# Kernel optimization log

Measured on AMD Instinct MI355X. Metric: run time of the kernel, lower is better.

The kernel has to match this reference:

```python
import jax, jax.numpy as jnp
from jax import lax
import numpy as np

D = 128          # condition_dim
NUM_STEPS = 1000
FFN = 2048       # torch TransformerEncoderLayer default dim_feedforward


def _conv(x, w, b):
    # 3x3 conv, stride 1, padding 1 (SAME), NCHW / OIHW layout as in torch
    y = lax.conv_general_dilated(x, w, (1, 1), 'SAME',
                                 dimension_numbers=('NCHW', 'OIHW', 'NCHW'))
    return y + b[None, :, None, None]


def _ln(x, g, b):
    m = jnp.mean(x, -1, keepdims=True)
    v = jnp.mean((x - m) ** 2, -1, keepdims=True)
    return (x - m) / jnp.sqrt(v + 1e-5) * g + b


def setup_inputs() -> dict:
    key = jax.random.key(0)
    ks = iter(jax.random.split(key, 40))
    B, C, H, W = 64, 3, 128, 128
    flat = C * H * W
    def rn(shape, scale=0.02):
        return jax.random.normal(next(ks), shape, jnp.float32) * scale
    return dict(
        cond_img=jax.random.normal(next(ks), (B, C, H, W), jnp.float32),
        tgt_img=jax.random.normal(next(ks), (B, C, H, W), jnp.float32),
        noise=jax.random.normal(next(ks), (B, C, H, W), jnp.float32),
        t=jax.random.randint(next(ks), (B,), 0, NUM_STEPS),
        # condition encoder params
        enc_lin_w=rn((D, flat)), enc_lin_b=jnp.zeros((D,), jnp.float32),
        in_w=rn((2, 3 * D, D)), in_b=jnp.zeros((2, 3 * D), jnp.float32),
        out_w=rn((2, D, D)), out_b=jnp.zeros((2, D), jnp.float32),
        ff1_w=rn((2, FFN, D)), ff1_b=jnp.zeros((2, FFN), jnp.float32),
        ff2_w=rn((2, D, FFN)), ff2_b=jnp.zeros((2, D), jnp.float32),
        ln1_g=jnp.ones((2, D), jnp.float32), ln1_b=jnp.zeros((2, D), jnp.float32),
        ln2_g=jnp.ones((2, D), jnp.float32), ln2_b=jnp.zeros((2, D), jnp.float32),
        # SimpleUNet params
        d1_w=rn((32, C, 3, 3)), d1_b=jnp.zeros((32,), jnp.float32),
        d2_w=rn((64, 32, 3, 3)), d2_b=jnp.zeros((64,), jnp.float32),
        mid_w=rn((64, D)), mid_b=jnp.zeros((64,), jnp.float32),
        u1_w=rn((32, 64, 3, 3)), u1_b=jnp.zeros((32,), jnp.float32),
        u2_w=rn((C, 32, 3, 3)), u2_b=jnp.zeros((C,), jnp.float32),
    )


def _forward(cond_img, tgt_img, noise, t,
             enc_lin_w, enc_lin_b, in_w, in_b, out_w, out_b,
             ff1_w, ff1_b, ff2_w, ff2_b, ln1_g, ln1_b, ln2_g, ln2_b,
             d1_w, d1_b, d2_w, d2_b, mid_w, mid_b, u1_w, u1_b, u2_w, u2_b):
    B = cond_img.shape[0]
    # ---- TransformerConditionEncoder (seq_len == 1, eval mode) ----
    x = cond_img.reshape(B, -1) @ enc_lin_w.T + enc_lin_b  # [B, D]
    for i in range(2):
        # self-attention over a length-1 sequence: softmax over one key == 1,
        # so attn(x) == out_proj(v_proj(x)) exactly.
        v = x @ in_w[i][2 * D:3 * D].T + in_b[i][2 * D:3 * D]
        a = v @ out_w[i].T + out_b[i]
        x = _ln(x + a, ln1_g[i], ln1_b[i])
        f = jnp.maximum(x @ ff1_w[i].T + ff1_b[i], 0.0) @ ff2_w[i].T + ff2_b[i]
        x = _ln(x + f, ln2_g[i], ln2_b[i])
    c = x  # [B, D]
    # ---- LinearScheduler.q_sample ----
    betas = jnp.linspace(1e-4, 0.02, NUM_STEPS)
    alpha_bars = jnp.cumprod(1.0 - betas)
    ab = alpha_bars[t][:, None, None, None]
    z_t = jnp.sqrt(ab) * tgt_img + jnp.sqrt(1.0 - ab) * noise
    # ---- SimpleUNet ----
    h = jax.nn.relu(_conv(z_t, d1_w, d1_b))
    h = jax.nn.relu(_conv(h, d2_w, d2_b))
    h = h + (c @ mid_w.T + mid_b)[:, :, None, None]
    h = jax.nn.relu(_conv(h, u1_w, u1_b))
    eps_pred = _conv(h, u2_w, u2_b)
    # ---- MSE loss ----
    return jnp.mean((eps_pred - noise) ** 2)


def reference(cond_img, tgt_img, noise, t,
              enc_lin_w, enc_lin_b, in_w, in_b, out_w, out_b,
              ff1_w, ff1_b, ff2_w, ff2_b, ln1_g, ln1_b, ln2_g, ln2_b,
              d1_w, d1_b, d2_w, d2_b, mid_w, mid_b, u1_w, u1_b, u2_w, u2_b):
    return _forward(cond_img, tgt_img, noise, t,
                    enc_lin_w, enc_lin_b, in_w, in_b, out_w, out_b,
                    ff1_w, ff1_b, ff2_w, ff2_b, ln1_g, ln1_b, ln2_g, ln2_b,
                    d1_w, d1_b, d2_w, d2_b, mid_w, mid_b, u1_w, u1_b, u2_w, u2_b)
```

## Files before the change

kernel.cpp:

```cpp
#include <hip/hip_runtime.h>
#include <math.h>

#define ENC_K 49152
#define KSEG 64
#define KLEN (ENC_K / KSEG)

typedef __attribute__((ext_vector_type(8))) short bf16x8;
typedef __attribute__((ext_vector_type(4))) float f32x4;

__device__ inline unsigned short f2bf(float f) {
    unsigned int u = __builtin_bit_cast(unsigned int, f);
    unsigned int r = u + 0x7fffu + ((u >> 16) & 1u);
    return (unsigned short)(r >> 16);
}
__device__ inline float bf2f(unsigned short h) {
    return __builtin_bit_cast(float, ((unsigned int)h) << 16);
}
__device__ inline float dot4(const float4 a, const float4 b) {
    return a.x * b.x + a.y * b.y + a.z * b.z + a.w * b.w;
}

__global__ void k_alpha(const int* __restrict__ t, float* __restrict__ sab, float* __restrict__ snab) {
    int b = threadIdx.x;
    if (b < 64) {
        int tb = t[b];
        const float step = (0.02f - 1e-4f) / 999.0f;
        float ab = 1.0f;
        for (int i = 0; i <= tb; ++i) {
            float beta = 1e-4f + step * (float)i;
            ab *= (1.0f - beta);
        }
        sab[b] = sqrtf(ab);
        snab[b] = sqrtf(1.0f - ab);
    }
}

__global__ void k_prep_cw(const float* __restrict__ w, unsigned short* __restrict__ out, int CO, int CI) {
    int idx = blockIdx.x * 256 + threadIdx.x;
    int total = CO * CI * 9;
    if (idx < total) {
        int tap = idx / (CO * CI);
        int rem = idx % (CO * CI);
        int co = rem / CI, ci = rem % CI;
        out[idx] = f2bf(w[((size_t)co * CI + ci) * 9 + tap]);
    }
}

__global__ void k_prep_u2(const float* __restrict__ w, unsigned short* __restrict__ out) {
    int idx = blockIdx.x * 256 + threadIdx.x;
    if (idx < 9 * 16 * 32) {
        int tap = idx / 512;
        int rem = idx % 512;
        int co = rem / 32, ci = rem % 32;
        out[idx] = (co < 3) ? f2bf(w[((size_t)co * 32 + ci) * 9 + tap]) : (unsigned short)0;
    }
}

__global__ void k_prep_bf(const float* __restrict__ in, unsigned short* __restrict__ out, int n) {
    int i = blockIdx.x * 256 + threadIdx.x;
    if (i < n) out[i] = f2bf(in[i]);
}

__global__ void k_enc_gemm(const float* __restrict__ cond, const float* __restrict__ w,
                           float* __restrict__ partial) {
    __shared__ float As[32][68];
    __shared__ float Ws[32][68];
    int tid = threadIdx.x;
    int j = tid & 15, i = tid >> 4;
    int d0 = blockIdx.x * 32, b0 = blockIdx.y * 32;
    int k0 = blockIdx.z * KLEN;
    float a00 = 0.f, a01 = 0.f, a10 = 0.f, a11 = 0.f;
    for (int kk = 0; kk < KLEN; kk += 64) {
        for (int idx = tid; idx < 512; idx += 256) {
            int r = idx >> 4, c = (idx & 15) << 2;
            *(float4*)&As[r][c] = *(const float4*)&cond[(size_t)(b0 + r) * ENC_K + k0 + kk + c];
            *(float4*)&Ws[r][c] = *(const float4*)&w[(size_t)(d0 + r) * ENC_K + k0 + kk + c];
        }
        __syncthreads();
        const float4* aA = (const float4*)&As[i][0];
        const float4* aB = (const float4*)&As[i + 16][0];
        const float4* wA = (const float4*)&Ws[j][0];
        const float4* wB = (const float4*)&Ws[j + 16][0];
#pragma unroll
        for (int k = 0; k < 16; ++k) {
            float4 av0 = aA[k], av1 = aB[k], wv0 = wA[k], wv1 = wB[k];
            a00 += dot4(av0, wv0); a01 += dot4(av0, wv1);
            a10 += dot4(av1, wv0); a11 += dot4(av1, wv1);
        }
        __syncthreads();
    }
    size_t base = (size_t)blockIdx.z * 64;
    partial[(base + b0 + i) * 128 + d0 + j] = a00;
    partial[(base + b0 + i) * 128 + d0 + j + 16] = a01;
    partial[(base + b0 + i + 16) * 128 + d0 + j] = a10;
    partial[(base + b0 + i + 16) * 128 + d0 + j + 16] = a11;
}

__global__ void k_enc_reduce(const float* __restrict__ partial, const float* __restrict__ bias,
                             float* __restrict__ x0) {
    int idx = blockIdx.x * 256 + threadIdx.x;
    float s = bias[idx & 127];
    for (int ks = 0; ks < KSEG; ++ks) s += partial[(size_t)ks * 8192 + idx];
    x0[idx] = s;
}

__device__ float sum128(float v, int tid, float* red) {
    if (tid < 128) red[tid] = v;
    __syncthreads();
    if (tid < 64) red[tid] += red[tid + 64]; __syncthreads();
    if (tid < 32) red[tid] += red[tid + 32]; __syncthreads();
    if (tid < 16) red[tid] += red[tid + 16]; __syncthreads();
    if (tid < 8)  red[tid] += red[tid + 8];  __syncthreads();
    if (tid < 4)  red[tid] += red[tid + 4];  __syncthreads();
    if (tid < 2)  red[tid] += red[tid + 2];  __syncthreads();
    if (tid < 1)  red[tid] += red[tid + 1];  __syncthreads();
    float s = red[0];
    __syncthreads();
    return s;
}

__global__ __launch_bounds__(512) void k_tf_attn(
    const float* __restrict__ xs, float* __restrict__ yo,
    const float* __restrict__ in_w, const float* __restrict__ in_b,
    const float* __restrict__ out_w, const float* __restrict__ out_b,
    const float* __restrict__ ln1_g, const float* __restrict__ ln1_b, int L) {
    __shared__ float xr[128], vr[128], tp[4][128], red[128];
    int b = blockIdx.x, tid = threadIdx.x;
    if (tid < 128) xr[tid] = xs[b * 128 + tid];
    __syncthreads();
    int d = tid & 127, s = tid >> 7;
    {
        const float4* w = (const float4*)(in_w + ((size_t)L * 384 + 256 + d) * 128) + s * 8;
        const float4* x4 = (const float4*)xr + s * 8;
        float p = 0.f;
#pragma unroll
        for (int k = 0; k < 8; ++k) p += dot4(x4[k], w[k]);
        tp[s][d] = p;
    }
    __syncthreads();
    if (tid < 128) vr[tid] = in_b[L * 384 + 256 + tid] + tp[0][tid] + tp[1][tid] + tp[2][tid] + tp[3][tid];
    __syncthreads();
    {
        const float4* w = (const float4*)(out_w + ((size_t)L * 128 + d) * 128) + s * 8;
        const float4* v4 = (const float4*)vr + s * 8;
        float p = 0.f;
#pragma unroll
        for (int k = 0; k < 8; ++k) p += dot4(v4[k], w[k]);
        tp[s][d] = p;
    }
    __syncthreads();
    float y = 0.f;
    if (tid < 128) y = xr[tid] + out_b[L * 128 + tid] + tp[0][tid] + tp[1][tid] + tp[2][tid] + tp[3][tid];
    float m1 = sum128(y, tid, red) * (1.f / 128.f);
    float c1 = y - m1;
    float v1 = sum128(c1 * c1, tid, red) * (1.f / 128.f);
    if (tid < 128)
        yo[b * 128 + tid] = c1 * rsqrtf(v1 + 1e-5f) * ln1_g[L * 128 + tid] + ln1_b[L * 128 + tid];
}

__global__ __launch_bounds__(256, 2) void k_ff1m(
    const float* __restrict__ yo, const unsigned short* __restrict__ w1b,
    const float* __restrict__ ff1_b, unsigned short* __restrict__ f1, int L) {
    __shared__ __align__(16) unsigned short xs[64 * 136];
    int tid = threadIdx.x;
    int lane = tid & 63, wv = tid >> 6, l15 = lane & 15, ch = lane >> 4;
    int n0 = blockIdx.x * 64 + wv * 16;
    for (int e = tid; e < 8192; e += 256)
        xs[(e >> 7) * 136 + (e & 127)] = f2bf(yo[e]);
    __syncthreads();
    f32x4 acc[4];
    f32x4 zf = {0.f, 0.f, 0.f, 0.f};
#pragma unroll
    for (int rg = 0; rg < 4; ++rg) acc[rg] = zf;
    const unsigned short* wrow = w1b + ((size_t)L * 2048 + n0 + l15) * 128 + ch * 8;
#pragma unroll
    for (int ks = 0; ks < 4; ++ks) {
        bf16x8 af = *(const bf16x8*)(wrow + ks * 32);
#pragma unroll
        for (int rg = 0; rg < 4; ++rg) {
            bf16x8 bv = *(const bf16x8*)(xs + (rg * 16 + l15) * 136 + ks * 32 + ch * 8);
            acc[rg] = __builtin_amdgcn_mfma_f32_16x16x32_bf16(af, bv, acc[rg], 0, 0, 0);
        }
    }
#pragma unroll
    for (int rg = 0; rg < 4; ++rg) {
        ushort4 o;
#pragma unroll
        for (int r = 0; r < 4; ++r)
            ((unsigned short*)&o)[r] =
                f2bf(fmaxf(acc[rg][r] + ff1_b[L * 2048 + n0 + ch * 4 + r], 0.f));
        *(ushort4*)(f1 + (size_t)(rg * 16 + l15) * 2056 + n0 + ch * 4) = o;
    }
}

__global__ __launch_bounds__(256, 2) void k_ff2m(
    const unsigned short* __restrict__ f1, const unsigned short* __restrict__ w2b,
    float* __restrict__ part, int L) {
    int tid = threadIdx.x;
    int lane = tid & 63, wv = tid >> 6, l15 = lane & 15, ch = lane >> 4;
    int ks = blockIdx.x;
    int dw = blockIdx.y * 64 + wv * 16;
    f32x4 acc[4];
    f32x4 zf = {0.f, 0.f, 0.f, 0.f};
#pragma unroll
    for (int rg = 0; rg < 4; ++rg) acc[rg] = zf;
    const unsigned short* wrow = w2b + ((size_t)L * 128 + dw + l15) * 2048 + ks * 512 + ch * 8;
    const unsigned short* frow = f1 + ks * 512 + ch * 8;
#pragma unroll
    for (int kst = 0; kst < 16; ++kst) {
        bf16x8 af = *(const bf16x8*)(wrow + kst * 32);
#pragma unroll
        for (int rg = 0; rg < 4; ++rg) {
            bf16x8 bv = *(const bf16x8*)(frow + (size_t)(rg * 16 + l15) * 2056 + kst * 32);
            acc[rg] = __builtin_amdgcn_mfma_f32_16x16x32_bf16(af, bv, acc[rg], 0, 0, 0);
        }
    }
#pragma unroll
    for (int rg = 0; rg < 4; ++rg)
        *(float4*)&part[((size_t)ks * 64 + rg * 16 + l15) * 128 + dw + ch * 4] = *(float4*)&acc[rg];
}

__global__ __launch_bounds__(128) void k_tf_red(
    const float* __restrict__ part, const float* __restrict__ yo,
    float* __restrict__ xs, const float* __restrict__ ff2_b,
    const float* __restrict__ ln2_g, const float* __restrict__ ln2_b, int L) {
    __shared__ float red[128];
    int b = blockIdx.x, tid = threadIdx.x;
    float y2 = yo[b * 128 + tid] + ff2_b[L * 128 + tid];
#pragma unroll
    for (int ks = 0; ks < 4; ++ks) y2 += part[((size_t)ks * 64 + b) * 128 + tid];
    float m2 = sum128(y2, tid, red) * (1.f / 128.f);
    float c2 = y2 - m2;
    float v2 = sum128(c2 * c2, tid, red) * (1.f / 128.f);
    xs[b * 128 + tid] = c2 * rsqrtf(v2 + 1e-5f) * ln2_g[L * 128 + tid] + ln2_b[L * 128 + tid];
}

__global__ void k_mid(const float* __restrict__ xe, const float* __restrict__ mid_w,
                      const float* __restrict__ mid_b, float* __restrict__ mid) {
    int b = blockIdx.x, c = threadIdx.x;
    float s = mid_b[c];
    const float* xr = xe + b * 128;
    const float* wr = mid_w + c * 128;
    for (int k = 0; k < 128; ++k) s += xr[k] * wr[k];
    mid[b * 64 + c] = s;
}

__global__ __launch_bounds__(256, 4) void k_conv1(
    const float* __restrict__ tgt, const float* __restrict__ noise,
    const float* __restrict__ sab, const float* __restrict__ snab,
    const float* __restrict__ wgt, const float* __restrict__ bias,
    unsigned short* __restrict__ h1, int b0) {
    __shared__ float it[3][34][35];
    __shared__ float wt[8][3][9];
    int tid = threadIdx.x;
    int tx = tid & 7, ty = tid >> 3;
    int bx = blockIdx.x, by = blockIdx.y;
    int bl = blockIdx.z >> 2, g = blockIdx.z & 3;
    int bg = b0 + bl, co0 = g * 8;
    float za = sab[bg], zb = snab[bg];
    for (int idx = tid; idx < 3 * 34 * 34; idx += 256) {
        int c = idx / 1156, rem = idx % 1156;
        int yy = rem / 34, xx = rem % 34;
        int gy = by * 32 + yy - 1, gx = bx * 32 + xx - 1;
        float v = 0.f;
        if (gy >= 0 && gy < 128 && gx >= 0 && gx < 128) {
            size_t off = (((size_t)bg * 3 + c) * 128 + gy) * 128 + gx;
            v = za * tgt[off] + zb * noise[off];
        }
        it[c][yy][xx] = v;
    }
    for (int idx = tid; idx < 8 * 27; idx += 256) {
        int co = idx / 27, rem = idx % 27;
        wt[co][rem / 9][rem % 9] = wgt[(size_t)(co0 + co) * 27 + rem];
    }
    __syncthreads();
    float acc[8][4];
#pragma unroll
    for (int co = 0; co < 8; ++co)
#pragma unroll
        for (int p = 0; p < 4; ++p) acc[co][p] = 0.f;
#pragma unroll
    for (int c = 0; c < 3; ++c)
#pragma unroll
        for (int ky = 0; ky < 3; ++ky) {
            float win[6];
#pragma unroll
            for (int i = 0; i < 6; ++i) win[i] = it[c][ty + ky][tx * 4 + i];
#pragma unroll
            for (int kx = 0; kx < 3; ++kx)
#pragma unroll
                for (int co = 0; co < 8; ++co) {
                    float w = wt[co][c][ky * 3 + kx];
#pragma unroll
                    for (int p = 0; p < 4; ++p) acc[co][p] += win[kx + p] * w;
                }
        }
    int gy = by * 32 + ty, gx0 = bx * 32 + tx * 4;
#pragma unroll
    for (int p = 0; p < 4; ++p) {
        ushort4 oa, ob;
#pragma unroll
        for (int co = 0; co < 4; ++co)
            ((unsigned short*)&oa)[co] = f2bf(fmaxf(acc[co][p] + bias[co0 + co], 0.f));
#pragma unroll
        for (int co = 0; co < 4; ++co)
            ((unsigned short*)&ob)[co] = f2bf(fmaxf(acc[co + 4][p] + bias[co0 + co + 4], 0.f));
        size_t o = (((size_t)bl * 128 + gy) * 128 + gx0 + p) * 32 + co0;
        *(ushort4*)(h1 + o) = oa;
        *(ushort4*)(h1 + o + 4) = ob;
    }
}

template <int CIN, int COUT, int MOUT>
__global__ __launch_bounds__(256, 4) void k_convR(
    const unsigned short* __restrict__ in, const unsigned short* __restrict__ wb,
    const float* __restrict__ bias, const float* __restrict__ mid,
    unsigned short* __restrict__ out, int b0) {
    const int GROUPS = COUT / 32;
    __shared__ __align__(16) unsigned short in_t[10 * 34 * 40];
    int tid = threadIdx.x;
    int bx = blockIdx.x, by = blockIdx.y;
    int bl = blockIdx.z / GROUPS, g = blockIdx.z % GROUPS;
    int bg = b0 + bl;
    int co0 = g * 32;
    int lane = tid & 63, wv = tid >> 6;
    int l15 = lane & 15, ch = lane >> 4;

    f32x4 acc[2][2][2];
    f32x4 zf = {0.f, 0.f, 0.f, 0.f};
#pragma unroll
    for (int a = 0; a < 2; ++a)
#pragma unroll
        for (int bq = 0; bq < 2; ++bq)
#pragma unroll
            for (int c = 0; c < 2; ++c) acc[a][bq][c] = zf;

    for (int cs = 0; cs < CIN / 32; ++cs) {
        if (cs) __syncthreads();
        for (int c = tid; c < 10 * 34 * 4; c += 256) {
            int cc = c & 3, pix = c >> 2;
            int xx = pix % 34, yy = pix / 34;
            int gy = by * 8 + yy - 1, gx = bx * 32 + xx - 1;
            bf16x8 v = {0, 0, 0, 0, 0, 0, 0, 0};
            if (gy >= 0 && gy < 128 && gx >= 0 && gx < 128)
                v = *(const bf16x8*)(in + (((size_t)bl * 128 + gy) * 128 + gx) * CIN + cs * 32 + cc * 8);
            *(bf16x8*)(in_t + pix * 40 + cc * 8) = v;
        }
        __syncthreads();
#pragma unroll
        for (int ky = 0; ky < 3; ++ky) {
            bf16x8 wreg[3][2];
#pragma unroll
            for (int kx = 0; kx < 3; ++kx)
#pragma unroll
                for (int cb = 0; cb < 2; ++cb)
                    wreg[kx][cb] = *(const bf16x8*)(
                        wb + ((size_t)((ky * 3 + kx) * COUT + co0 + cb * 16 + l15)) * CIN + cs * 32 + ch * 8);
#pragma unroll
            for (int kx = 0; kx < 3; ++kx) {
#pragma unroll
                for (int yl = 0; yl < 2; ++yl) {
                    int yloc = 2 * wv + yl + ky;
#pragma unroll
                    for (int xt = 0; xt < 2; ++xt) {
                        int xloc = xt * 16 + l15 + kx;
                        bf16x8 bfv = *(const bf16x8*)(in_t + (yloc * 34 + xloc) * 40 + ch * 8);
#pragma unroll
                        for (int cb = 0; cb < 2; ++cb)
                            acc[yl][xt][cb] = __builtin_amdgcn_mfma_f32_16x16x32_bf16(
                                wreg[kx][cb], bfv, acc[yl][xt][cb], 0, 0, 0);
                    }
                }
            }
        }
    }
#pragma unroll
    for (int yl = 0; yl < 2; ++yl) {
        int gy = by * 8 + 2 * wv + yl;
#pragma unroll
        for (int xt = 0; xt < 2; ++xt) {
            int gx = bx * 32 + xt * 16 + l15;
            size_t pixo = (((size_t)bl * 128 + gy) * 128 + gx) * COUT;
#pragma unroll
            for (int cb = 0; cb < 2; ++cb) {
                int co = co0 + cb * 16 + ch * 4;
                ushort4 o;
#pragma unroll
                for (int r = 0; r < 4; ++r) {
                    float v = acc[yl][xt][cb][r] + bias[co + r];
                    v = fmaxf(v, 0.f);
                    if (MOUT == 2) v += mid[bg * 64 + co + r];
                    ((unsigned short*)&o)[r] = f2bf(v);
                }
                *(ushort4*)(out + pixo + co) = o;
            }
        }
    }
}

__global__ __launch_bounds__(256, 3) void k_u2m(
    const unsigned short* __restrict__ h3, const unsigned short* __restrict__ wbu2,
    const float* __restrict__ u2_b, const float* __restrict__ noise,
    float* __restrict__ partial, int b0) {
    __shared__ __align__(16) unsigned short in_t[340 * 40];
    __shared__ __align__(16) unsigned short w_t[9 * 16 * 40];
    __shared__ float rs[256];
    int tid = threadIdx.x;
    int bx = blockIdx.x, by = blockIdx.y, bl = blockIdx.z;
    int bg = b0 + bl;
    int lane = tid & 63, wv = tid >> 6, l15 = lane & 15, ch = lane >> 4;

    for (int c = tid; c < 340 * 4; c += 256) {
        int cc = c & 3, pix = c >> 2;
        int xx = pix % 34, yy = pix / 34;
        int gy = by * 8 + yy - 1, gx = bx * 32 + xx - 1;
        bf16x8 v = {0, 0, 0, 0, 0, 0, 0, 0};
        if (gy >= 0 && gy < 128 && gx >= 0 && gx < 128)
            v = *(const bf16x8*)(h3 + (((size_t)bl * 128 + gy) * 128 + gx) * 32 + cc * 8);
        *(bf16x8*)(in_t + pix * 40 + cc * 8) = v;
    }
    for (int c = tid; c < 9 * 16 * 4; c += 256) {
        int cc = c & 3, row = c >> 2;
        bf16x8 v = *(const bf16x8*)(wbu2 + (size_t)row * 32 + cc * 8);
        *(bf16x8*)(w_t + row * 40 + cc * 8) = v;
    }
    __syncthreads();

    f32x4 acc[2][2];
    f32x4 zf = {0.f, 0.f, 0.f, 0.f};
    acc[0][0] = zf; acc[0][1] = zf; acc[1][0] = zf; acc[1][1] = zf;
#pragma unroll
    for (int ky = 0; ky < 3; ++ky)
#pragma unroll
        for (int kx = 0; kx < 3; ++kx) {
            int tap = ky * 3 + kx;
            bf16x8 af = *(const bf16x8*)(w_t + (tap * 16 + l15) * 40 + ch * 8);
#pragma unroll
            for (int yl = 0; yl < 2; ++yl) {
                int yloc = 2 * wv + yl + ky;
#pragma unroll
                for (int xt = 0; xt < 2; ++xt) {
                    int xloc = xt * 16 + l15 + kx;
                    bf16x8 bfv = *(const bf16x8*)(in_t + (yloc * 34 + xloc) * 40 + ch * 8);
                    acc[yl][xt] = __builtin_amdgcn_mfma_f32_16x16x32_bf16(af, bfv, acc[yl][xt], 0, 0, 0);
                }
            }
        }
    float ss = 0.f;
    if (ch == 0) {
#pragma unroll
        for (int yl = 0; yl < 2; ++yl) {
            int gy = by * 8 + 2 * wv + yl;
#pragma unroll
            for (int xt = 0; xt < 2; ++xt) {
                int gx = bx * 32 + xt * 16 + l15;
#pragma unroll
                for (int r = 0; r < 3; ++r) {
                    float v = acc[yl][xt][r] + u2_b[r];
                    float d = v - noise[(((size_t)bg * 3 + r) * 128 + gy) * 128 + gx];
                    ss += d * d;
                }
            }
        }
    }
    rs[tid] = ss;
    __syncthreads();
    for (int s = 128; s > 0; s >>= 1) {
        if (tid < s) rs[tid] += rs[tid + s];
        __syncthreads();
    }
    if (tid == 0) partial[bg * 64 + by * 4 + bx] = rs[0];
}

__global__ void k_final(const float* __restrict__ partial, float* __restrict__ out) {
    __shared__ float rs[256];
    int tid = threadIdx.x;
    float s = 0.f;
    for (int i = tid; i < 4096; i += 256) s += partial[i];
    rs[tid] = s;
    __syncthreads();
    for (int st = 128; st > 0; st >>= 1) {
        if (tid < st) rs[tid] += rs[tid + st];
        __syncthreads();
    }
    if (tid == 0) out[0] = rs[0] / 3145728.0f;
}

extern "C" void kernel_launch(void* const* d_in, const int* in_sizes, int n_in,
                              void* d_out, int out_size, void* d_ws, size_t ws_size,
                              hipStream_t stream) {
    const float* cond   = (const float*)d_in[0];
    const float* tgt    = (const float*)d_in[1];
    const float* noise  = (const float*)d_in[2];
    const int*   t      = (const int*)d_in[3];
    const float* enc_w  = (const float*)d_in[4];
    const float* enc_b  = (const float*)d_in[5];
    const float* in_w   = (const float*)d_in[6];
    const float* in_b   = (const float*)d_in[7];
    const float* out_w  = (const float*)d_in[8];
    const float* out_b  = (const float*)d_in[9];
    const float* ff1_w  = (const float*)d_in[10];
    const float* ff1_b  = (const float*)d_in[11];
    const float* ff2_w  = (const float*)d_in[12];
    const float* ff2_b  = (const float*)d_in[13];
    const float* ln1_g  = (const float*)d_in[14];
    const float* ln1_b  = (const float*)d_in[15];
    const float* ln2_g  = (const float*)d_in[16];
    const float* ln2_b  = (const float*)d_in[17];
    const float* d1_w   = (const float*)d_in[18];
    const float* d1_b   = (const float*)d_in[19];
    const float* d2_w   = (const float*)d_in[20];
    const float* d2_b   = (const float*)d_in[21];
    const float* mid_w  = (const float*)d_in[22];
    const float* mid_b  = (const float*)d_in[23];
    const float* u1_w   = (const float*)d_in[24];
    const float* u1_b   = (const float*)d_in[25];
    const float* u2_w   = (const float*)d_in[26];
    const float* u2_b   = (const float*)d_in[27];

    float* ws = (float*)d_ws;
    float* sab     = ws;
    float* snab    = ws + 64;
    float* x0      = ws + 128;
    float* mid     = ws + 16512;
    float* msepart = ws + 86144;
    unsigned short* wb2  = (unsigned short*)(ws + 90240);
    unsigned short* wbu1 = (unsigned short*)(ws + 99456);
    unsigned short* wbu2 = (unsigned short*)(ws + 108672);

    const size_t SMALL = 131072;
    const size_t ENCP = (size_t)KSEG * 8192;
    float* encpart = ws + SMALL;
    float* tfy     = encpart + ENCP;
    unsigned short* tff1 = (unsigned short*)(tfy + 8192);
    float* tfpart  = tfy + 8192 + 65792;
    unsigned short* wbf1 = (unsigned short*)(tfpart + 32768);
    unsigned short* wbf2 = (unsigned short*)(tfpart + 32768 + 262144);

    size_t fixed = SMALL + ENCP + 8192 + 65792 + 32768 + 262144 + 262144;
    size_t avail = (ws_size / 4 > fixed) ? (ws_size / 4 - fixed) : 0;
    int NB = 1;
    const int cands[7] = {64, 32, 16, 8, 4, 2, 1};
    for (int ci = 0; ci < 7; ++ci) {
        if ((size_t)cands[ci] * 1048576ull <= avail) { NB = cands[ci]; break; }
    }
    unsigned short* hb1 = (unsigned short*)(ws + fixed);
    unsigned short* hb2 = (unsigned short*)(ws + fixed + (size_t)NB * 262144ull);
    unsigned short* hb3 = (unsigned short*)(ws + fixed + (size_t)NB * 786432ull);

    k_alpha<<<1, 64, 0, stream>>>(t, sab, snab);
    k_prep_cw<<<72, 256, 0, stream>>>(d2_w, wb2, 64, 32);
    k_prep_cw<<<72, 256, 0, stream>>>(u1_w, wbu1, 32, 64);
    k_prep_u2<<<18, 256, 0, stream>>>(u2_w, wbu2);
    k_prep_bf<<<2048, 256, 0, stream>>>(ff1_w, wbf1, 524288);
    k_prep_bf<<<2048, 256, 0, stream>>>(ff2_w, wbf2, 524288);
    k_enc_gemm<<<dim3(4, 2, KSEG), 256, 0, stream>>>(cond, enc_w, encpart);
    k_enc_reduce<<<32, 256, 0, stream>>>(encpart, enc_b, x0);
    for (int L = 0; L < 2; ++L) {
        k_tf_attn<<<64, 512, 0, stream>>>(x0, tfy, in_w, in_b, out_w, out_b, ln1_g, ln1_b, L);
        k_ff1m<<<32, 256, 0, stream>>>(tfy, wbf1, ff1_b, tff1, L);
        k_ff2m<<<dim3(4, 2), 256, 0, stream>>>(tff1, wbf2, tfpart, L);
        k_tf_red<<<64, 128, 0, stream>>>(tfpart, tfy, x0, ff2_b, ln2_g, ln2_b, L);
    }
    k_mid<<<64, 64, 0, stream>>>(x0, mid_w, mid_b, mid);

    for (int cb = 0; cb < 64; cb += NB) {
        k_conv1<<<dim3(4, 4, NB * 4), 256, 0, stream>>>(
            tgt, noise, sab, snab, d1_w, d1_b, hb1, cb);
        k_convR<32, 64, 2><<<dim3(4, 16, NB * 2), 256, 0, stream>>>(
            hb1, wb2, d2_b, mid, hb2, cb);
        k_convR<64, 32, 1><<<dim3(4, 16, NB), 256, 0, stream>>>(
            hb2, wbu1, u1_b, nullptr, hb3, cb);
        k_u2m<<<dim3(4, 16, NB), 256, 0, stream>>>(
            hb3, wbu2, u2_b, noise, msepart, cb);
    }

    k_final<<<1, 256, 0, stream>>>(msepart, (float*)d_out);
}
```

Baseline: 448.4 us.

## Fuse d2 and u1 convolutions into one kernel with shared-memory intermediate

Replaces the two separate k_convR launches (d2 conv with mid add, then u1 conv) with a single kernel. It computes the 64-channel d2 output for an 8x32 tile plus a 1-pixel halo into LDS, in two 32-channel halves, and feeds each half straight into the u1 conv accumulators. This drops the 64-channel h2 activation buffer's global write and read and frees workspace, allowing a larger batch chunk. The cost is redundant halo computation for d2, more LDS per block with lower occupancy (launch bounds 3), and an LDS row stride of 34 shorts that may cause misaligned 16-byte accesses.

```diff
diff --git a/kernel.cpp b/kernel.cpp
--- a/kernel.cpp
+++ b/kernel.cpp
@@ -311,89 +311,110 @@
     }
 }
 
-template <int CIN, int COUT, int MOUT>
-__global__ __launch_bounds__(256, 4) void k_convR(
-    const unsigned short* __restrict__ in, const unsigned short* __restrict__ wb,
-    const float* __restrict__ bias, const float* __restrict__ mid,
-    unsigned short* __restrict__ out, int b0) {
-    const int GROUPS = COUT / 32;
-    __shared__ __align__(16) unsigned short in_t[10 * 34 * 40];
-    int tid = threadIdx.x;
-    int bx = blockIdx.x, by = blockIdx.y;
-    int bl = blockIdx.z / GROUPS, g = blockIdx.z % GROUPS;
+__global__ __launch_bounds__(256, 3) void k_fuse21(
+    const unsigned short* __restrict__ h1, const unsigned short* __restrict__ wb2,
+    const float* __restrict__ d2_b, const float* __restrict__ mid,
+    const unsigned short* __restrict__ wbu1, const float* __restrict__ u1_b,
+    unsigned short* __restrict__ h3, int b0) {
+    __shared__ __align__(16) unsigned short h1t[432 * 34];
+    __shared__ __align__(16) unsigned short h2t[340 * 34];
+    int tid = threadIdx.x;
+    int bx = blockIdx.x, by = blockIdx.y, bl = blockIdx.z;
     int bg = b0 + bl;
-    int co0 = g * 32;
-    int lane = tid & 63, wv = tid >> 6;
-    int l15 = lane & 15, ch = lane >> 4;
-
-    f32x4 acc[2][2][2];
+    int lane = tid & 63, wv = tid >> 6, l15 = lane & 15, ch = lane >> 4;
+
+    for (int idx = tid; idx < 432 * 4; idx += 256) {
+        int cc = idx & 3, p = idx >> 2;
+        int r = p / 36, c = p % 36;
+        int gy = by * 8 + r - 2, gx = bx * 32 + c - 2;
+        bf16x8 v = {0, 0, 0, 0, 0, 0, 0, 0};
+        if (gy >= 0 && gy < 128 && gx >= 0 && gx < 128)
+            v = *(const bf16x8*)(h1 + (((size_t)bl * 128 + gy) * 128 + gx) * 32 + cc * 8);
+        *(bf16x8*)(h1t + p * 34 + cc * 8) = v;
+    }
+    __syncthreads();
+
     f32x4 zf = {0.f, 0.f, 0.f, 0.f};
-#pragma unroll
-    for (int a = 0; a < 2; ++a)
-#pragma unroll
-        for (int bq = 0; bq < 2; ++bq)
-#pragma unroll
-            for (int c = 0; c < 2; ++c) acc[a][bq][c] = zf;
-
-    for (int cs = 0; cs < CIN / 32; ++cs) {
-        if (cs) __syncthreads();
-        for (int c = tid; c < 10 * 34 * 4; c += 256) {
-            int cc = c & 3, pix = c >> 2;
-            int xx = pix % 34, yy = pix / 34;
-            int gy = by * 8 + yy - 1, gx = bx * 32 + xx - 1;
-            bf16x8 v = {0, 0, 0, 0, 0, 0, 0, 0};
-            if (gy >= 0 && gy < 128 && gx >= 0 && gx < 128)
-                v = *(const bf16x8*)(in + (((size_t)bl * 128 + gy) * 128 + gx) * CIN + cs * 32 + cc * 8);
-            *(bf16x8*)(in_t + pix * 40 + cc * 8) = v;
-        }
-        __syncthreads();
-#pragma unroll
-        for (int ky = 0; ky < 3; ++ky) {
-            bf16x8 wreg[3][2];
-#pragma unroll
-            for (int kx = 0; kx < 3; ++kx)
-#pragma unroll
-                for (int cb = 0; cb < 2; ++cb)
-                    wreg[kx][cb] = *(const bf16x8*)(
-                        wb + ((size_t)((ky * 3 + kx) * COUT + co0 + cb * 16 + l15)) * CIN + cs * 32 + ch * 8);
-#pragma unroll
-            for (int kx = 0; kx < 3; ++kx) {
-#pragma unroll
-                for (int yl = 0; yl < 2; ++yl) {
-                    int yloc = 2 * wv + yl + ky;
-#pragma unroll
-                    for (int xt = 0; xt < 2; ++xt) {
-                        int xloc = xt * 16 + l15 + kx;
-                        bf16x8 bfv = *(const bf16x8*)(in_t + (yloc * 34 + xloc) * 40 + ch * 8);
-#pragma unroll
-                        for (int cb = 0; cb < 2; ++cb)
-                            acc[yl][xt][cb] = __builtin_amdgcn_mfma_f32_16x16x32_bf16(
-                                wreg[kx][cb], bfv, acc[yl][xt][cb], 0, 0, 0);
-                    }
+    f32x4 uacc[4][2];
+#pragma unroll
+    for (int k = 0; k < 4; ++k) { uacc[k][0] = zf; uacc[k][1] = zf; }
+
+    for (int h = 0; h < 2; ++h) {
+        if (h) __syncthreads();
+        f32x4 aacc[6][2];
+#pragma unroll
+        for (int k = 0; k < 6; ++k) { aacc[k][0] = zf; aacc[k][1] = zf; }
+#pragma unroll
+        for (int tap = 0; tap < 9; ++tap) {
+            int ky = tap / 3, kx = tap % 3;
+            bf16x8 A0 = *(const bf16x8*)(wb2 + ((size_t)(tap * 64 + h * 32 + l15)) * 32 + ch * 8);
+            bf16x8 A1 = *(const bf16x8*)(wb2 + ((size_t)(tap * 64 + h * 32 + 16 + l15)) * 32 + ch * 8);
+#pragma unroll
+            for (int k = 0; k < 6; ++k) {
+                int grp = wv + 4 * k;
+                if (grp < 22) {
+                    int pl = grp * 16 + l15;
+                    int plc = pl < 340 ? pl : 339;
+                    int r2 = plc / 34, c2 = plc % 34;
+                    bf16x8 B = *(const bf16x8*)(h1t + ((r2 + ky) * 36 + (c2 + kx)) * 34 + ch * 8);
+                    aacc[k][0] = __builtin_amdgcn_mfma_f32_16x16x32_bf16(A0, B, aacc[k][0], 0, 0, 0);
+                    aacc[k][1] = __builtin_amdgcn_mfma_f32_16x16x32_bf16(A1, B, aacc[k][1], 0, 0, 0);
                 }
             }
         }
-    }
-#pragma unroll
-    for (int yl = 0; yl < 2; ++yl) {
-        int gy = by * 8 + 2 * wv + yl;
-#pragma unroll
-        for (int xt = 0; xt < 2; ++xt) {
-            int gx = bx * 32 + xt * 16 + l15;
-            size_t pixo = (((size_t)bl * 128 + gy) * 128 + gx) * COUT;
-#pragma unroll
-            for (int cb = 0; cb < 2; ++cb) {
-                int co = co0 + cb * 16 + ch * 4;
-                ushort4 o;
-#pragma unroll
-                for (int r = 0; r < 4; ++r) {
-                    float v = acc[yl][xt][cb][r] + bias[co + r];
-                    v = fmaxf(v, 0.f);
-                    if (MOUT == 2) v += mid[bg * 64 + co + r];
-                    ((unsigned short*)&o)[r] = f2bf(v);
+#pragma unroll
+        for (int k = 0; k < 6; ++k) {
+            int grp = wv + 4 * k;
+            if (grp < 22) {
+                int pl = grp * 16 + l15;
+                bool pv = pl < 340;
+                int plc = pv ? pl : 339;
+                int r2 = plc / 34, c2 = plc % 34;
+                int gy2 = by * 8 + r2 - 1, gx2 = bx * 32 + c2 - 1;
+                bool inimg = pv && gy2 >= 0 && gy2 < 128 && gx2 >= 0 && gx2 < 128;
+#pragma unroll
+                for (int cb = 0; cb < 2; ++cb) {
+                    int co = h * 32 + cb * 16 + ch * 4;
+                    ushort4 o;
+#pragma unroll
+                    for (int r = 0; r < 4; ++r) {
+                        float v = fmaxf(aacc[k][cb][r] + d2_b[co + r], 0.f) + mid[bg * 64 + co + r];
+                        ((unsigned short*)&o)[r] = inimg ? f2bf(v) : (unsigned short)0;
+                    }
+                    if (pv) *(ushort4*)(h2t + plc * 34 + cb * 16 + ch * 4) = o;
                 }
-                *(ushort4*)(out + pixo + co) = o;
             }
+        }
+        __syncthreads();
+#pragma unroll
+        for (int tap = 0; tap < 9; ++tap) {
+            int ky = tap / 3, kx = tap % 3;
+            bf16x8 A0 = *(const bf16x8*)(wbu1 + ((size_t)(tap * 32 + l15)) * 64 + h * 32 + ch * 8);
+            bf16x8 A1 = *(const bf16x8*)(wbu1 + ((size_t)(tap * 32 + 16 + l15)) * 64 + h * 32 + ch * 8);
+#pragma unroll
+            for (int k = 0; k < 4; ++k) {
+                int pl = (wv + 4 * k) * 16 + l15;
+                int r3 = pl / 32, c3 = pl % 32;
+                bf16x8 B = *(const bf16x8*)(h2t + ((r3 + ky) * 34 + (c3 + kx)) * 34 + ch * 8);
+                uacc[k][0] = __builtin_amdgcn_mfma_f32_16x16x32_bf16(A0, B, uacc[k][0], 0, 0, 0);
+                uacc[k][1] = __builtin_amdgcn_mfma_f32_16x16x32_bf16(A1, B, uacc[k][1], 0, 0, 0);
+            }
+        }
+    }
+#pragma unroll
+    for (int k = 0; k < 4; ++k) {
+        int pl = (wv + 4 * k) * 16 + l15;
+        int r3 = pl / 32, c3 = pl % 32;
+        int gy = by * 8 + r3, gx = bx * 32 + c3;
+        size_t pixo = (((size_t)bl * 128 + gy) * 128 + gx) * 32;
+#pragma unroll
+        for (int cb = 0; cb < 2; ++cb) {
+            int co = cb * 16 + ch * 4;
+            ushort4 o;
+#pragma unroll
+            for (int r = 0; r < 4; ++r)
+                ((unsigned short*)&o)[r] = f2bf(fmaxf(uacc[k][cb][r] + u1_b[co + r], 0.f));
+            *(ushort4*)(h3 + pixo + co) = o;
         }
     }
 }
@@ -542,11 +563,10 @@
     int NB = 1;
     const int cands[7] = {64, 32, 16, 8, 4, 2, 1};
     for (int ci = 0; ci < 7; ++ci) {
-        if ((size_t)cands[ci] * 1048576ull <= avail) { NB = cands[ci]; break; }
+        if ((size_t)cands[ci] * 524288ull <= avail) { NB = cands[ci]; break; }
     }
     unsigned short* hb1 = (unsigned short*)(ws + fixed);
-    unsigned short* hb2 = (unsigned short*)(ws + fixed + (size_t)NB * 262144ull);
-    unsigned short* hb3 = (unsigned short*)(ws + fixed + (size_t)NB * 786432ull);
+    unsigned short* hb3 = (unsigned short*)(ws + fixed + (size_t)NB * 262144ull);
 
     k_alpha<<<1, 64, 0, stream>>>(t, sab, snab);
     k_prep_cw<<<72, 256, 0, stream>>>(d2_w, wb2, 64, 32);
@@ -567,10 +587,8 @@
     for (int cb = 0; cb < 64; cb += NB) {
         k_conv1<<<dim3(4, 4, NB * 4), 256, 0, stream>>>(
             tgt, noise, sab, snab, d1_w, d1_b, hb1, cb);
-        k_convR<32, 64, 2><<<dim3(4, 16, NB * 2), 256, 0, stream>>>(
-            hb1, wb2, d2_b, mid, hb2, cb);
-        k_convR<64, 32, 1><<<dim3(4, 16, NB), 256, 0, stream>>>(
-            hb2, wbu1, u1_b, nullptr, hb3, cb);
+        k_fuse21<<<dim3(4, 16, NB), 256, 0, stream>>>(
+            hb1, wb2, d2_b, mid, wbu1, u1_b, hb3, cb);
         k_u2m<<<dim3(4, 16, NB), 256, 0, stream>>>(
             hb3, wbu2, u2_b, noise, msepart, cb);
     }
```

Measured after the change: 662.0 us. 47.6% more time.
